# Kernel tuning notes

Measured on AMD Instinct MI355X. Metric: run time of the kernel, lower is better.

Reference implementation:

```python
import jax, jax.numpy as jnp
import numpy as np

HIDDEN = 1024
HEADS = 16
HEAD_DIM = HIDDEN // HEADS
SCALE = HEAD_DIM ** (-0.5)


def setup_inputs() -> dict:
    key = jax.random.key(0)
    ks = jax.random.split(key, 5)
    B, N, C = 8, 1024, HIDDEN
    x = jax.random.normal(ks[0], (B, N, C), dtype=jnp.float32)
    # torch nn.Linear params: weight [out, in], bias [out]
    w_in = jax.random.normal(ks[1], (3 * C, C), dtype=jnp.float32) * (C ** -0.5)
    b_in = jax.random.normal(ks[2], (3 * C,), dtype=jnp.float32) * 0.02
    w_out = jax.random.normal(ks[3], (C, C), dtype=jnp.float32) * (C ** -0.5)
    b_out = jax.random.normal(ks[4], (C,), dtype=jnp.float32) * 0.02
    return {"x": x, "w_in": w_in, "b_in": b_in, "w_out": w_out, "b_out": b_out}


def reference(x, w_in, b_in, w_out, b_out):
    B, N, C = x.shape
    H, D = HEADS, HEAD_DIM
    # in_proj: [B,N,3C] -> (3,B,H,N,D)
    qkv = x @ w_in.T + b_in
    qkv = qkv.reshape(B, N, 3, H, D).transpose(2, 0, 3, 1, 4)
    q, k, v = qkv[0], qkv[1], qkv[2]
    # attention scores scaled after QK^T (same math as scaling q)
    attn = jnp.einsum("bhnd,bhmd->bhnm", q, k) * SCALE
    attn = jax.nn.softmax(attn, axis=-1)
    out = jnp.einsum("bhnm,bhmd->bhnd", attn, v)  # [B,H,N,D]
    out = out.transpose(0, 2, 1, 3).reshape(B, N, C)
    return out @ w_out.T + b_out
```

## Files before the change

kernel.cpp:

```cpp
#include <hip/hip_runtime.h>


typedef __attribute__((ext_vector_type(8))) __bf16 bf16x8;
typedef __attribute__((ext_vector_type(4))) __bf16 bf16x4;
typedef __attribute__((ext_vector_type(4))) float f32x4;
typedef __attribute__((ext_vector_type(4))) short short4v;

__device__ __forceinline__ f32x4 mfma16(bf16x8 a, bf16x8 b, f32x4 c) {
  return __builtin_amdgcn_mfma_f32_16x16x32_bf16(a, b, c, 0, 0, 0);
}

#if __has_builtin(__builtin_amdgcn_mfma_f32_16x16x16bf16_1k)
__device__ __forceinline__ f32x4 mfma_pv(bf16x4 a, bf16x4 b, f32x4 c) {
  short4v as = __builtin_bit_cast(short4v, a);
  short4v bs = __builtin_bit_cast(short4v, b);
  return __builtin_amdgcn_mfma_f32_16x16x16bf16_1k(as, bs, c, 0, 0, 0);
}
#else
__device__ __forceinline__ f32x4 mfma_pv(bf16x4 a, bf16x4 b, f32x4 c) {
  __bf16 z = (__bf16)0.f;
  bf16x8 a8 = {a[0], a[1], a[2], a[3], z, z, z, z};
  bf16x8 b8 = {b[0], b[1], b[2], b[3], z, z, z, z};
  return mfma16(a8, b8, c);
}
#endif

__device__ __forceinline__ float fexp2(float x) {
#if __has_builtin(__builtin_amdgcn_exp2f)
  return __builtin_amdgcn_exp2f(x);
#else
  return exp2f(x);
#endif
}

typedef __attribute__((address_space(1))) const unsigned int gu32;
typedef __attribute__((address_space(3))) unsigned int lu32;

__device__ __forceinline__ void async16(const void* g, void* l) {
  __builtin_amdgcn_global_load_lds((gu32*)g, (lu32*)l, 16, 0, 0);
}

__global__ __launch_bounds__(256) void cvt_kernel(const float* __restrict__ in,
                                                  __bf16* __restrict__ out, int n) {
  int i = (blockIdx.x * 256 + threadIdx.x) * 8;
  if (i >= n) return;
  float4 a = *(const float4*)(in + i);
  float4 b = *(const float4*)(in + i + 4);
  bf16x8 o;
  o[0] = (__bf16)a.x; o[1] = (__bf16)a.y; o[2] = (__bf16)a.z; o[3] = (__bf16)a.w;
  o[4] = (__bf16)b.x; o[5] = (__bf16)b.y; o[6] = (__bf16)b.z; o[7] = (__bf16)b.w;
  *(bf16x8*)(out + i) = o;
}

template <typename OutT>
__global__ __launch_bounds__(256) void gemm_nt(const __bf16* __restrict__ A,
                                               const __bf16* __restrict__ Bm,
                                               const float* __restrict__ bias,
                                               OutT* __restrict__ C, int K, int ldc) {
  __shared__ __bf16 As[128 * 32];
  __shared__ __bf16 Bs[128 * 32];
  const int t = threadIdx.x;
  const int wv = t >> 6, lane = t & 63;
  const int q16 = lane & 15, quad = lane >> 4;
  const int wm = wv >> 1, wn = wv & 1;
  const long m0 = (long)blockIdx.x * 128;
  const long n0 = (long)blockIdx.y * 128;

  f32x4 zero = {0.f, 0.f, 0.f, 0.f};
  f32x4 acc[4][4];
#pragma unroll
  for (int i = 0; i < 4; ++i)
#pragma unroll
    for (int j = 0; j < 4; ++j) acc[i][j] = zero;

  char* AsB = (char*)As;
  char* BsB = (char*)Bs;
  const int sr = t >> 2;
  const int cs = t & 3;
  const int gc = cs ^ ((sr >> 1) & 3);

  for (int kt = 0; kt < K; kt += 32) {
    __syncthreads();
    async16(A + (m0 + sr) * K + kt + gc * 8,      AsB + wv * 1024);
    async16(A + (m0 + 64 + sr) * K + kt + gc * 8, AsB + 4096 + wv * 1024);
    async16(Bm + (n0 + sr) * K + kt + gc * 8,      BsB + wv * 1024);
    async16(Bm + (n0 + 64 + sr) * K + kt + gc * 8, BsB + 4096 + wv * 1024);
    __syncthreads();

    bf16x8 af[4], bf[4];
#pragma unroll
    for (int i = 0; i < 4; ++i) {
      int ra = wm * 64 + i * 16 + q16;
      af[i] = *(const bf16x8*)(AsB + ra * 64 + ((quad ^ ((ra >> 1) & 3)) * 16));
      int rb = wn * 64 + i * 16 + q16;
      bf[i] = *(const bf16x8*)(BsB + rb * 64 + ((quad ^ ((rb >> 1) & 3)) * 16));
    }
#pragma unroll
    for (int i = 0; i < 4; ++i)
#pragma unroll
      for (int j = 0; j < 4; ++j) acc[i][j] = mfma16(af[i], bf[j], acc[i][j]);
  }

#pragma unroll
  for (int j = 0; j < 4; ++j) {
    long col = n0 + wn * 64 + j * 16 + q16;
    float bs = bias[col];
#pragma unroll
    for (int i = 0; i < 4; ++i) {
      long rowb = m0 + wm * 64 + i * 16 + quad * 4;
#pragma unroll
      for (int r = 0; r < 4; ++r) {
        float v = acc[i][j][r] + bs;
        C[(rowb + r) * (long)ldc + col] = (OutT)v;
      }
    }
  }
}

__global__ __launch_bounds__(256) void vtrans_kernel(const __bf16* __restrict__ qkv,
                                                     __bf16* __restrict__ vt) {
  __shared__ __bf16 L[64 * 72];
  const int t = threadIdx.x;
  const int bh = blockIdx.x;
  const int b = bh >> 4, h = bh & 15;
  const int n0 = blockIdx.y * 64;
  const long rowbase = (long)b * 1024 + n0;

#pragma unroll
  for (int p = 0; p < 2; ++p) {
    int unit = p * 256 + t;
    int row = unit >> 3, c = unit & 7;
    bf16x8 v = *(const bf16x8*)(qkv + (rowbase + row) * 3072 + 2048 + h * 64 + c * 8);
#pragma unroll
    for (int j = 0; j < 8; ++j) L[(c * 8 + j) * 72 + row] = v[j];
  }
  __syncthreads();
#pragma unroll
  for (int p = 0; p < 2; ++p) {
    int unit = p * 256 + t;
    int d = unit >> 3, c = unit & 7;
    bf16x8 v = *(const bf16x8*)(L + d * 72 + c * 8);
    *(bf16x8*)(vt + (long)bh * 65536 + (long)d * 1024 + n0 + c * 8) = v;
  }
}

__global__ __launch_bounds__(256) void attn_kernel(const __bf16* __restrict__ qkv,
                                                   const __bf16* __restrict__ vt,
                                                   __bf16* __restrict__ ao) {
  __shared__ __bf16 Ks[64 * 64];
  __shared__ __bf16 Vt[64 * 64];
  const int t = threadIdx.x;
  const int wv = t >> 6, lane = t & 63;
  const int q16 = lane & 15, quad = lane >> 4;
  const int bh = blockIdx.x;
  const int b = bh >> 4, h = bh & 15;
  const int q0 = blockIdx.y * 64;
  const long rowbase = (long)b * 1024;

  bf16x8 qf0, qf1;
  {
    long qrow = rowbase + q0 + wv * 16 + q16;
    const __bf16* qp = qkv + qrow * 3072 + h * 64 + quad * 8;
    qf0 = *(const bf16x8*)qp;
    qf1 = *(const bf16x8*)(qp + 32);
#pragma unroll
    for (int j = 0; j < 8; ++j) {
      qf0[j] = (__bf16)((float)qf0[j] * 0.18033688f);
      qf1[j] = (__bf16)((float)qf1[j] * 0.18033688f);
    }
  }

  f32x4 zero = {0.f, 0.f, 0.f, 0.f};
  f32x4 oacc[4];
#pragma unroll
  for (int dt = 0; dt < 4; ++dt) oacc[dt] = zero;
  float lcol = 0.f;

  char* KsB = (char*)Ks;
  char* VtB = (char*)Vt;
  const int sr = t >> 3;
  const int sgc = (t & 7) ^ (sr & 7);
  const int sw = q16 & 7;

  for (int kv0 = 0; kv0 < 1024; kv0 += 64) {
    __syncthreads();
    const __bf16* kg = qkv + (rowbase + kv0 + sr) * 3072 + 1024 + h * 64 + sgc * 8;
    async16(kg, KsB + wv * 1024);
    async16(kg + (long)32 * 3072, KsB + 4096 + wv * 1024);
    const __bf16* vg = vt + (long)bh * 65536 + (long)sr * 1024 + kv0 + sgc * 8;
    async16(vg, VtB + wv * 1024);
    async16(vg + (long)32 * 1024, VtB + 4096 + wv * 1024);
    __syncthreads();

    f32x4 sacc[4];
#pragma unroll
    for (int nt = 0; nt < 4; ++nt) sacc[nt] = zero;
#pragma unroll
    for (int nt = 0; nt < 4; ++nt) {
      int kvr = nt * 16 + q16;
      bf16x8 kf0 = *(const bf16x8*)(KsB + kvr * 128 + ((quad ^ sw) * 16));
      bf16x8 kf1 = *(const bf16x8*)(KsB + kvr * 128 + (((4 + quad) ^ sw) * 16));
      sacc[nt] = mfma16(kf0, qf0, sacc[nt]);
      sacc[nt] = mfma16(kf1, qf1, sacc[nt]);
    }

    bf16x4 pf[4];
#pragma unroll
    for (int nt = 0; nt < 4; ++nt)
#pragma unroll
      for (int r = 0; r < 4; ++r) {
        float p = fexp2(sacc[nt][r]);
        lcol += p;
        pf[nt][r] = (__bf16)p;
      }

#pragma unroll
    for (int nt = 0; nt < 4; ++nt) {
      int c = ((nt * 2 + (quad >> 1)) ^ sw) * 16 + (quad & 1) * 8;
#pragma unroll
      for (int dt = 0; dt < 4; ++dt) {
        bf16x4 vf = *(const bf16x4*)(VtB + (dt * 16 + q16) * 128 + c);
        oacc[dt] = mfma_pv(pf[nt], vf, oacc[dt]);
      }
    }
  }

  lcol += __shfl_xor(lcol, 16);
  lcol += __shfl_xor(lcol, 32);
  float inv = 1.0f / lcol;
#pragma unroll
  for (int r = 0; r < 4; ++r) {
    float ir = __shfl(inv, quad * 4 + r);
    long orow = rowbase + q0 + wv * 16 + quad * 4 + r;
#pragma unroll
    for (int dt = 0; dt < 4; ++dt)
      ao[orow * 1024 + h * 64 + dt * 16 + q16] = (__bf16)(oacc[dt][r] * ir);
  }
}

extern "C" void kernel_launch(void* const* d_in, const int* in_sizes, int n_in,
                              void* d_out, int out_size, void* d_ws, size_t ws_size,
                              hipStream_t stream) {
  const float* x     = (const float*)d_in[0];
  const float* w_in  = (const float*)d_in[1];
  const float* b_in  = (const float*)d_in[2];
  const float* w_out = (const float*)d_in[3];
  const float* b_out = (const float*)d_in[4];
  float* out = (float*)d_out;

  char* ws = (char*)d_ws;
  __bf16* xb   = (__bf16*)(ws);
  __bf16* vtg  = (__bf16*)(ws);
  __bf16* wib  = (__bf16*)(ws + 16777216);
  __bf16* wob  = (__bf16*)(ws + 23068672);
  __bf16* qkvb = (__bf16*)(ws + 25165824);
  __bf16* aob  = (__bf16*)(ws + 75497472);

  cvt_kernel<<<4096, 256, 0, stream>>>(x, xb, 8388608);
  cvt_kernel<<<1536, 256, 0, stream>>>(w_in, wib, 3145728);
  cvt_kernel<<<512, 256, 0, stream>>>(w_out, wob, 1048576);

  gemm_nt<__bf16><<<dim3(64, 24), 256, 0, stream>>>(xb, wib, b_in, qkvb, 1024, 3072);
  vtrans_kernel<<<dim3(128, 16), 256, 0, stream>>>(qkvb, vtg);
  attn_kernel<<<dim3(128, 16), 256, 0, stream>>>(qkvb, vtg, aob);
  gemm_nt<float><<<dim3(64, 8), 256, 0, stream>>>(aob, wob, b_out, out, 1024, 1024);
}
```

Baseline: 259.9 us.

## Fuse V transpose into QKV GEMM epilogue, widen tile, merge convert launches

The QKV projection GEMM now writes the V part straight into the transposed per-head layout from its epilogue, so the separate vtrans kernel and its extra pass over V are gone. The transposed V buffer moves into the output buffer, which is only written later by the final GEMM. The QKV GEMM also uses a wider N tile (256 columns per block, 8 MFMA column tiles per wave) with a launch-bounds occupancy hint. The three fp32-to-bf16 conversion launches are merged into one. The trade-offs are higher register pressure from the wider tile and narrower, strided bf16x4 stores in the V epilogue.

```diff
diff --git a/kernel.cpp b/kernel.cpp
--- a/kernel.cpp
+++ b/kernel.cpp
@@ -40,10 +40,20 @@
   __builtin_amdgcn_global_load_lds((gu32*)g, (lu32*)l, 16, 0, 0);
 }
 
-__global__ __launch_bounds__(256) void cvt_kernel(const float* __restrict__ in,
-                                                  __bf16* __restrict__ out, int n) {
-  int i = (blockIdx.x * 256 + threadIdx.x) * 8;
-  if (i >= n) return;
+__global__ __launch_bounds__(256) void cvt_all(const float* __restrict__ x,
+                                               __bf16* __restrict__ xb,
+                                               const float* __restrict__ wi,
+                                               __bf16* __restrict__ wib,
+                                               const float* __restrict__ wo,
+                                               __bf16* __restrict__ wob) {
+  int blk = blockIdx.x;
+  const float* in;
+  __bf16* out;
+  int base;
+  if (blk < 4096)      { in = x;  out = xb;  base = 0; }
+  else if (blk < 5632) { in = wi; out = wib; base = 4096; }
+  else                 { in = wo; out = wob; base = 5632; }
+  int i = ((blk - base) * 256 + threadIdx.x) * 8;
   float4 a = *(const float4*)(in + i);
   float4 b = *(const float4*)(in + i + 4);
   bf16x8 o;
@@ -52,26 +62,27 @@
   *(bf16x8*)(out + i) = o;
 }
 
-template <typename OutT>
-__global__ __launch_bounds__(256) void gemm_nt(const __bf16* __restrict__ A,
-                                               const __bf16* __restrict__ Bm,
-                                               const float* __restrict__ bias,
-                                               OutT* __restrict__ C, int K, int ldc) {
+template <int NB, bool WRITE_VT, typename OutT>
+__global__ __launch_bounds__(256, 2) void gemm_nt(const __bf16* __restrict__ A,
+                                                  const __bf16* __restrict__ Bm,
+                                                  const float* __restrict__ bias,
+                                                  OutT* __restrict__ C, int K, int ldc,
+                                                  __bf16* __restrict__ vt) {
   __shared__ __bf16 As[128 * 32];
-  __shared__ __bf16 Bs[128 * 32];
+  __shared__ __bf16 Bs[NB * 64 * 32];
   const int t = threadIdx.x;
   const int wv = t >> 6, lane = t & 63;
   const int q16 = lane & 15, quad = lane >> 4;
   const int wm = wv >> 1, wn = wv & 1;
   const long m0 = (long)blockIdx.x * 128;
-  const long n0 = (long)blockIdx.y * 128;
+  const long n0 = (long)blockIdx.y * (NB * 32);
 
   f32x4 zero = {0.f, 0.f, 0.f, 0.f};
-  f32x4 acc[4][4];
+  f32x4 acc[4][NB];
 #pragma unroll
   for (int i = 0; i < 4; ++i)
 #pragma unroll
-    for (int j = 0; j < 4; ++j) acc[i][j] = zero;
+    for (int j = 0; j < NB; ++j) acc[i][j] = zero;
 
   char* AsB = (char*)As;
   char* BsB = (char*)Bs;
@@ -83,64 +94,62 @@
     __syncthreads();
     async16(A + (m0 + sr) * K + kt + gc * 8,      AsB + wv * 1024);
     async16(A + (m0 + 64 + sr) * K + kt + gc * 8, AsB + 4096 + wv * 1024);
-    async16(Bm + (n0 + sr) * K + kt + gc * 8,      BsB + wv * 1024);
-    async16(Bm + (n0 + 64 + sr) * K + kt + gc * 8, BsB + 4096 + wv * 1024);
-    __syncthreads();
-
-    bf16x8 af[4], bf[4];
+#pragma unroll
+    for (int s = 0; s < NB / 2; ++s)
+      async16(Bm + (n0 + s * 64 + sr) * K + kt + gc * 8, BsB + s * 4096 + wv * 1024);
+    __syncthreads();
+
+    bf16x8 af[4], bf[NB];
 #pragma unroll
     for (int i = 0; i < 4; ++i) {
       int ra = wm * 64 + i * 16 + q16;
       af[i] = *(const bf16x8*)(AsB + ra * 64 + ((quad ^ ((ra >> 1) & 3)) * 16));
-      int rb = wn * 64 + i * 16 + q16;
-      bf[i] = *(const bf16x8*)(BsB + rb * 64 + ((quad ^ ((rb >> 1) & 3)) * 16));
+    }
+#pragma unroll
+    for (int j = 0; j < NB; ++j) {
+      int rb = wn * (NB * 16) + j * 16 + q16;
+      bf[j] = *(const bf16x8*)(BsB + rb * 64 + ((quad ^ ((rb >> 1) & 3)) * 16));
     }
 #pragma unroll
     for (int i = 0; i < 4; ++i)
 #pragma unroll
-      for (int j = 0; j < 4; ++j) acc[i][j] = mfma16(af[i], bf[j], acc[i][j]);
-  }
-
-#pragma unroll
-  for (int j = 0; j < 4; ++j) {
-    long col = n0 + wn * 64 + j * 16 + q16;
-    float bs = bias[col];
-#pragma unroll
-    for (int i = 0; i < 4; ++i) {
-      long rowb = m0 + wm * 64 + i * 16 + quad * 4;
-#pragma unroll
-      for (int r = 0; r < 4; ++r) {
-        float v = acc[i][j][r] + bs;
-        C[(rowb + r) * (long)ldc + col] = (OutT)v;
-      }
-    }
-  }
-}
-
-__global__ __launch_bounds__(256) void vtrans_kernel(const __bf16* __restrict__ qkv,
-                                                     __bf16* __restrict__ vt) {
-  __shared__ __bf16 L[64 * 72];
-  const int t = threadIdx.x;
-  const int bh = blockIdx.x;
-  const int b = bh >> 4, h = bh & 15;
-  const int n0 = blockIdx.y * 64;
-  const long rowbase = (long)b * 1024 + n0;
-
-#pragma unroll
-  for (int p = 0; p < 2; ++p) {
-    int unit = p * 256 + t;
-    int row = unit >> 3, c = unit & 7;
-    bf16x8 v = *(const bf16x8*)(qkv + (rowbase + row) * 3072 + 2048 + h * 64 + c * 8);
-#pragma unroll
-    for (int j = 0; j < 8; ++j) L[(c * 8 + j) * 72 + row] = v[j];
-  }
-  __syncthreads();
-#pragma unroll
-  for (int p = 0; p < 2; ++p) {
-    int unit = p * 256 + t;
-    int d = unit >> 3, c = unit & 7;
-    bf16x8 v = *(const bf16x8*)(L + d * 72 + c * 8);
-    *(bf16x8*)(vt + (long)bh * 65536 + (long)d * 1024 + n0 + c * 8) = v;
+      for (int j = 0; j < NB; ++j) acc[i][j] = mfma16(af[i], bf[j], acc[i][j]);
+  }
+
+  if (WRITE_VT && n0 >= 2048) {
+    const int b = (int)(m0 >> 10);
+    const int nbase = (int)(m0 - (long)b * 1024) + wm * 64;
+#pragma unroll
+    for (int j = 0; j < NB; ++j) {
+      int col = (int)n0 + wn * (NB * 16) + j * 16 + q16;
+      int cc = col - 2048;
+      int h = cc >> 6, d = cc & 63;
+      float bs = bias[col];
+      __bf16* vrow = vt + (((long)(b * 16 + h)) << 16) + (long)d * 1024;
+#pragma unroll
+      for (int i = 0; i < 4; ++i) {
+        int n = nbase + i * 16 + quad * 4;
+        bf16x4 o;
+#pragma unroll
+        for (int r = 0; r < 4; ++r) o[r] = (__bf16)(acc[i][j][r] + bs);
+        *(bf16x4*)(vrow + n) = o;
+      }
+    }
+  } else {
+#pragma unroll
+    for (int j = 0; j < NB; ++j) {
+      long col = n0 + wn * (NB * 16) + j * 16 + q16;
+      float bs = bias[col];
+#pragma unroll
+      for (int i = 0; i < 4; ++i) {
+        long rowb = m0 + wm * 64 + i * 16 + quad * 4;
+#pragma unroll
+        for (int r = 0; r < 4; ++r) {
+          float v = acc[i][j][r] + bs;
+          C[(rowb + r) * (long)ldc + col] = (OutT)v;
+        }
+      }
+    }
   }
 }
 
@@ -250,18 +259,16 @@
 
   char* ws = (char*)d_ws;
   __bf16* xb   = (__bf16*)(ws);
-  __bf16* vtg  = (__bf16*)(ws);
   __bf16* wib  = (__bf16*)(ws + 16777216);
   __bf16* wob  = (__bf16*)(ws + 23068672);
   __bf16* qkvb = (__bf16*)(ws + 25165824);
   __bf16* aob  = (__bf16*)(ws + 75497472);
-
-  cvt_kernel<<<4096, 256, 0, stream>>>(x, xb, 8388608);
-  cvt_kernel<<<1536, 256, 0, stream>>>(w_in, wib, 3145728);
-  cvt_kernel<<<512, 256, 0, stream>>>(w_out, wob, 1048576);
-
-  gemm_nt<__bf16><<<dim3(64, 24), 256, 0, stream>>>(xb, wib, b_in, qkvb, 1024, 3072);
-  vtrans_kernel<<<dim3(128, 16), 256, 0, stream>>>(qkvb, vtg);
+  __bf16* vtg  = (__bf16*)d_out;
+
+  cvt_all<<<6144, 256, 0, stream>>>(x, xb, w_in, wib, w_out, wob);
+  gemm_nt<8, true, __bf16><<<dim3(64, 12), 256, 0, stream>>>(
+      xb, wib, b_in, qkvb, 1024, 3072, vtg);
   attn_kernel<<<dim3(128, 16), 256, 0, stream>>>(qkvb, vtg, aob);
-  gemm_nt<float><<<dim3(64, 8), 256, 0, stream>>>(aob, wob, b_out, out, 1024, 1024);
-}
+  gemm_nt<4, false, float><<<dim3(64, 8), 256, 0, stream>>>(
+      aob, wob, b_out, out, 1024, 1024, nullptr);
+}
```

Result: faster. 253.9 us (-2.3%).
